# Kernel tuning notes

Measured on AMD Instinct MI355X. Metric: run time of the kernel, lower is better.

The kernel has to match this reference:

```python
import jax, jax.numpy as jnp
import numpy as np

HIDDEN = 1024
VOCAB = 32000
MAX_LENGTH = 30
SOS_TOKEN = 0


def setup_inputs() -> dict:
    key = jax.random.key(0)
    ks = jax.random.split(key, 10)
    B = 64
    s = 1.0 / np.sqrt(HIDDEN)
    return {
        "encoder_outputs": jax.random.normal(ks[0], (B, MAX_LENGTH, HIDDEN), jnp.float32),
        "encoder_hidden": jax.random.normal(ks[1], (1, B, HIDDEN), jnp.float32),
        "target_tensor": jax.random.randint(ks[2], (B, MAX_LENGTH), 0, VOCAB),
        "embedding": jax.random.normal(ks[3], (VOCAB, HIDDEN), jnp.float32),
        "w_ih": jax.random.uniform(ks[4], (3 * HIDDEN, HIDDEN), jnp.float32, -s, s),
        "w_hh": jax.random.uniform(ks[5], (3 * HIDDEN, HIDDEN), jnp.float32, -s, s),
        "b_ih": jax.random.uniform(ks[6], (3 * HIDDEN,), jnp.float32, -s, s),
        "b_hh": jax.random.uniform(ks[7], (3 * HIDDEN,), jnp.float32, -s, s),
        "out_w": jax.random.uniform(ks[8], (VOCAB, HIDDEN), jnp.float32, -s, s),
        "out_b": jax.random.uniform(ks[9], (VOCAB,), jnp.float32, -s, s),
    }


def reference(encoder_outputs, encoder_hidden, target_tensor, embedding,
              w_ih, w_hh, b_ih, b_hh, out_w, out_b):
    B = encoder_outputs.shape[0]
    h0 = encoder_hidden[0]  # [B, H]
    # teacher forcing: step i consumes SOS for i=0, else target[:, i-1]
    sos = jnp.full((B, 1), SOS_TOKEN, dtype=target_tensor.dtype)
    tokens = jnp.concatenate([sos, target_tensor[:, :-1]], axis=1).T  # [T, B]

    def step(h, tok):
        x = jax.nn.relu(embedding[tok])            # [B, H] (dropout = identity in eval)
        gi = x @ w_ih.T + b_ih                     # [B, 3H]
        gh = h @ w_hh.T + b_hh                     # [B, 3H]
        i_r, i_z, i_n = jnp.split(gi, 3, axis=-1)
        h_r, h_z, h_n = jnp.split(gh, 3, axis=-1)
        r = jax.nn.sigmoid(i_r + h_r)
        z = jax.nn.sigmoid(i_z + h_z)
        n = jnp.tanh(i_n + r * h_n)
        h_new = (1.0 - z) * n + z * h
        logits = h_new @ out_w.T + out_b           # [B, V]
        return h_new, logits

    h_final, logits = jax.lax.scan(step, h0, tokens)   # logits: [T, B, V]
    log_probs = jax.nn.log_softmax(logits.transpose(1, 0, 2), axis=-1)  # [B, T, V]
    return log_probs, h_final[None]  # hidden as [1, B, H]
```

## Files before the change

### kernel.cpp

```cpp
#include <hip/hip_runtime.h>
#include <math.h>

#define T_STEPS 30
#define BATCH   64
#define HID     1024
#define VOCABN  32000
#define G3      3072
#define ROWS    (T_STEPS * BATCH)
#define ROWS_PAD 2048
#define OUT_HID_OFF ((size_t)BATCH * T_STEPS * VOCABN)

typedef __attribute__((ext_vector_type(8))) short bf16x8;
typedef __attribute__((ext_vector_type(4))) float f32x4;

__device__ __forceinline__ unsigned short f2bf(float f) {
    union { float f; unsigned u; } x; x.f = f;
    unsigned r = x.u + 0x7fffu + ((x.u >> 16) & 1u);
    return (unsigned short)(r >> 16);
}
__device__ __forceinline__ float bf2f(unsigned short u) {
    union { unsigned u; float f; } x; x.u = (unsigned)u << 16;
    return x.f;
}

__device__ __forceinline__ void gld_lds16(const unsigned short* g, unsigned short* l) {
    __builtin_amdgcn_global_load_lds(
        (const __attribute__((address_space(1))) unsigned*)g,
        (__attribute__((address_space(3))) unsigned*)l, 16, 0, 0);
}

__global__ __launch_bounds__(256) void f32_to_bf16(const float* __restrict__ src,
                                                   unsigned short* __restrict__ dst, int n4) {
    int i = blockIdx.x * 256 + threadIdx.x;
    int stride = gridDim.x * 256;
    for (; i < n4; i += stride) {
        float4 v = ((const float4*)src)[i];
        ushort4 o;
        o.x = f2bf(v.x); o.y = f2bf(v.y); o.z = f2bf(v.z); o.w = f2bf(v.w);
        ((ushort4*)dst)[i] = o;
    }
}

__global__ __launch_bounds__(256) void embed_relu_bf16(const int* __restrict__ target,
                                                       const float* __restrict__ emb,
                                                       unsigned short* __restrict__ X) {
    int bid = blockIdx.x;
    int t = bid >> 6, b = bid & 63;
    int tok = (t == 0) ? 0 : target[b * T_STEPS + (t - 1)];
    const float4* src = (const float4*)(emb + (size_t)tok * HID);
    float4 v = src[threadIdx.x];
    ushort4 o;
    o.x = f2bf(fmaxf(v.x, 0.f)); o.y = f2bf(fmaxf(v.y, 0.f));
    o.z = f2bf(fmaxf(v.z, 0.f)); o.w = f2bf(fmaxf(v.w, 0.f));
    ((ushort4*)(X + (size_t)bid * HID))[threadIdx.x] = o;
}

__global__ void init_bar(unsigned int* bar) {
    if (threadIdx.x < 64) bar[threadIdx.x] = 0u;
}

__global__ __launch_bounds__(256) void gemm_mfma_bt(const unsigned short* __restrict__ A,
                                                    const unsigned short* __restrict__ W,
                                                    const float* __restrict__ bias,
                                                    float* __restrict__ out,
                                                    int N, int K) {
    __shared__ unsigned short As[128 * 64];
    __shared__ unsigned short Bs[128 * 64];
    int tid  = threadIdx.x;
    int lane = tid & 63;
    int wid  = tid >> 6;
    int wm   = wid >> 1, wn = wid & 1;
    const int bM = blockIdx.y * 128;
    const int bN = blockIdx.x * 128;

    f32x4 acc[4][4];
#pragma unroll
    for (int i = 0; i < 4; ++i)
#pragma unroll
        for (int j = 0; j < 4; ++j) acc[i][j] = (f32x4){0.f, 0.f, 0.f, 0.f};

    int sr[4], sc[4];
#pragma unroll
    for (int q = 0; q < 4; ++q) {
        sr[q] = (wid * 4 + q) * 8 + (lane >> 3);
        sc[q] = (lane & 7) ^ (sr[q] & 7);
    }

    for (int kt = 0; kt < K; kt += 64) {
        __syncthreads();
#pragma unroll
        for (int q = 0; q < 4; ++q) {
            gld_lds16(A + (size_t)(bM + sr[q]) * K + kt + sc[q] * 8, As + (wid * 4 + q) * 512);
            gld_lds16(W + (size_t)(bN + sr[q]) * K + kt + sc[q] * 8, Bs + (wid * 4 + q) * 512);
        }
        __syncthreads();

#pragma unroll
        for (int ks = 0; ks < 2; ++ks) {
            bf16x8 a[4], b[4];
#pragma unroll
            for (int mf = 0; mf < 4; ++mf) {
                int r  = wm * 64 + mf * 16 + (lane & 15);
                int ch = (ks * 4 + (lane >> 4)) ^ (r & 7);
                a[mf] = *(const bf16x8*)(As + r * 64 + ch * 8);
            }
#pragma unroll
            for (int nf = 0; nf < 4; ++nf) {
                int r  = wn * 64 + nf * 16 + (lane & 15);
                int ch = (ks * 4 + (lane >> 4)) ^ (r & 7);
                b[nf] = *(const bf16x8*)(Bs + r * 64 + ch * 8);
            }
#pragma unroll
            for (int mf = 0; mf < 4; ++mf)
#pragma unroll
                for (int nf = 0; nf < 4; ++nf)
                    acc[mf][nf] = __builtin_amdgcn_mfma_f32_16x16x32_bf16(
                        a[mf], b[nf], acc[mf][nf], 0, 0, 0);
        }
    }

    int rif = (lane >> 4) * 4;
    int col = lane & 15;
#pragma unroll
    for (int mf = 0; mf < 4; ++mf) {
#pragma unroll
        for (int j = 0; j < 4; ++j) {
            int gr = bM + wm * 64 + mf * 16 + rif + j;
#pragma unroll
            for (int nf = 0; nf < 4; ++nf) {
                int gc = bN + wn * 64 + nf * 16 + col;
                out[(size_t)gr * N + gc] = acc[mf][nf][j] + bias[gc];
            }
        }
    }
}

template <bool BF16OUT>
__global__ __launch_bounds__(512) void gemm_logits256(const unsigned short* __restrict__ A,
                                                      const unsigned short* __restrict__ W,
                                                      const float* __restrict__ bias,
                                                      float* __restrict__ out,
                                                      unsigned short* __restrict__ scratch) {
    __shared__ unsigned short As[2][256 * 32];
    __shared__ unsigned short Bs[2][256 * 32];
    int d   = blockIdx.x;
    int xcd = d & 7;
    int mt  = (d >> 3) & 7;
    int pg  = d >> 6;
    int p   = pg * 8 + xcd;
    if (p >= VOCABN / 256) return;
    const int bM = mt * 256;
    const int bN = p * 256;

    int tid  = threadIdx.x;
    int lane = tid & 63;
    int wid  = tid >> 6;
    int wm   = wid >> 2;
    int wn   = wid & 3;
    int l15  = lane & 15, l4 = lane >> 4;

    size_t pA[2], pB[2];
    int ldst[2];
#pragma unroll
    for (int i = 0; i < 2; ++i) {
        int c = wid * 128 + i * 64 + lane;
        int r = c >> 2, cc = c & 3;
        int so = (cc ^ ((r >> 1) & 3)) * 8;
        pA[i] = (size_t)(bM + r) * HID + so;
        pB[i] = (size_t)(bN + r) * HID + so;
        ldst[i] = wid * 1024 + i * 512;
    }

    f32x4 acc[8][4];
#pragma unroll
    for (int i = 0; i < 8; ++i)
#pragma unroll
        for (int j = 0; j < 4; ++j) acc[i][j] = (f32x4){0.f, 0.f, 0.f, 0.f};

    int chsw = (l4 ^ ((l15 >> 1) & 3)) * 8;
    int aoff[8], boff[4];
#pragma unroll
    for (int mf = 0; mf < 8; ++mf) aoff[mf] = (wm * 128 + mf * 16 + l15) * 32 + chsw;
#pragma unroll
    for (int nf = 0; nf < 4; ++nf) boff[nf] = (wn * 64 + nf * 16 + l15) * 32 + chsw;

    auto issue = [&](int s) {
        int slot = s & 1;
#pragma unroll
        for (int i = 0; i < 2; ++i)
            gld_lds16(A + pA[i] + s * 32, &As[slot][ldst[i]]);
#pragma unroll
        for (int i = 0; i < 2; ++i)
            gld_lds16(W + pB[i] + s * 32, &Bs[slot][ldst[i]]);
    };

    issue(0); issue(1);

#pragma unroll 1
    for (int s = 0; s < 32; ++s) {
        if (s < 31) asm volatile("s_waitcnt vmcnt(4)" ::: "memory");
        else        asm volatile("s_waitcnt vmcnt(0)" ::: "memory");
        __builtin_amdgcn_s_barrier();
        asm volatile("" ::: "memory");
        __builtin_amdgcn_sched_barrier(0);

        int slot = s & 1;
        const unsigned short* ab = As[slot];
        const unsigned short* bb = Bs[slot];
        bf16x8 a[8], b[4];
#pragma unroll
        for (int mf = 0; mf < 8; ++mf) a[mf] = *(const bf16x8*)(ab + aoff[mf]);
#pragma unroll
        for (int nf = 0; nf < 4; ++nf) b[nf] = *(const bf16x8*)(bb + boff[nf]);
        __builtin_amdgcn_s_setprio(1);
#pragma unroll
        for (int mf = 0; mf < 8; ++mf)
#pragma unroll
            for (int nf = 0; nf < 4; ++nf)
                acc[mf][nf] = __builtin_amdgcn_mfma_f32_16x16x32_bf16(
                    a[mf], b[nf], acc[mf][nf], 0, 0, 0);
        __builtin_amdgcn_s_setprio(0);

        asm volatile("s_waitcnt lgkmcnt(0)" ::: "memory");
        __builtin_amdgcn_s_barrier();
        asm volatile("" ::: "memory");
        __builtin_amdgcn_sched_barrier(0);
        if (s < 30) issue(s + 2);
    }

    int col = l15;
    float b4[4];
#pragma unroll
    for (int nf = 0; nf < 4; ++nf) b4[nf] = bias[bN + wn * 64 + nf * 16 + col];
    int rif = l4 * 4;
#pragma unroll
    for (int mf = 0; mf < 8; ++mf) {
#pragma unroll
        for (int j = 0; j < 4; ++j) {
            int gr = bM + wm * 128 + mf * 16 + rif + j;
            if (gr < ROWS) {
                int t = gr >> 6, b_ = gr & 63;
                size_t rowoff = ((size_t)b_ * T_STEPS + t) * (size_t)VOCABN;
#pragma unroll
                for (int nf = 0; nf < 4; ++nf) {
                    float v = acc[mf][nf][j] + b4[nf];
                    int gc = bN + wn * 64 + nf * 16 + col;
                    if (BF16OUT) scratch[rowoff + gc] = f2bf(v);
                    else         out[rowoff + gc] = v;
                }
            }
        }
    }
}

__global__ __launch_bounds__(256, 1) void gru_persistent(
    const unsigned short* __restrict__ h0b,
    const float* __restrict__ enc_h,
    const unsigned short* __restrict__ Whh,
    const float* __restrict__ b_hh,
    const float* __restrict__ gi,
    unsigned short* __restrict__ Hall,
    float* __restrict__ h_final,
    unsigned int* __restrict__ flags,
    const float* __restrict__ outw_f32,
    unsigned short* __restrict__ outw_bf)
{
    __shared__ unsigned short Wlds[48 * 1024];
    int tid  = threadIdx.x;

    if (blockIdx.x >= 64) {
        const int n4 = VOCABN * HID / 4;
        int i = (blockIdx.x - 64) * 256 + tid;
        const int stride = 192 * 256;
        for (; i < n4; i += stride) {
            float4 v = ((const float4*)outw_f32)[i];
            ushort4 o;
            o.x = f2bf(v.x); o.y = f2bf(v.y); o.z = f2bf(v.z); o.w = f2bf(v.w);
            ((ushort4*)outw_bf)[i] = o;
        }
        return;
    }

    int lane = tid & 63;
    int wq   = tid >> 6;
    int l15  = lane & 15, l4 = lane >> 4;
    int m0   = blockIdx.x * 16;
    int b    = wq * 16 + l15;
    int mb   = m0 + l4 * 4;

    for (int i = 0; i < 24; ++i) {
        int sb = wq * 24 + i;
        int kt = sb / 3, g = sb % 3;
        const unsigned short* src =
            Whh + (size_t)(g * HID + m0 + l15) * HID + kt * 32 + l4 * 8;
        gld_lds16(src, Wlds + sb * 512);
    }

    float hp[4];
    {
        float4 h4 = *(const float4*)(enc_h + (size_t)b * HID + mb);
        hp[0] = h4.x; hp[1] = h4.y; hp[2] = h4.z; hp[3] = h4.w;
    }
    float bhr[4], bhz[4], bhn[4];
    {
        float4 r4 = *(const float4*)(b_hh + mb);
        float4 z4 = *(const float4*)(b_hh + HID + mb);
        float4 n4 = *(const float4*)(b_hh + 2 * HID + mb);
        bhr[0]=r4.x; bhr[1]=r4.y; bhr[2]=r4.z; bhr[3]=r4.w;
        bhz[0]=z4.x; bhz[1]=z4.y; bhz[2]=z4.z; bhz[3]=z4.w;
        bhn[0]=n4.x; bhn[1]=n4.y; bhn[2]=n4.z; bhn[3]=n4.w;
    }
    __syncthreads();

    int arow16 = b * 128 + l4;

    for (int t = 0; t < T_STEPS; ++t) {
        const float* gib = gi + (size_t)t * BATCH * G3 + (size_t)b * G3;
        float4 giR = *(const float4*)(gib + mb);
        float4 giZ = *(const float4*)(gib + HID + mb);
        float4 giN = *(const float4*)(gib + 2 * HID + mb);
        float gr4[4] = {giR.x, giR.y, giR.z, giR.w};
        float gz4[4] = {giZ.x, giZ.y, giZ.z, giZ.w};
        float gn4[4] = {giN.x, giN.y, giN.z, giN.w};

        if (t > 0) {
            if (tid < 64) {
                while (__hip_atomic_load(flags + tid, __ATOMIC_RELAXED,
                                         __HIP_MEMORY_SCOPE_AGENT) < (unsigned)t) {}
            }
            __builtin_amdgcn_sched_barrier(0);
            __syncthreads();
            asm volatile("" ::: "memory");
        }

        const unsigned short* Asrc = (t == 0) ? h0b : (Hall + (size_t)(t - 1) * BATCH * HID);
        const bf16x8* A16 = (const bf16x8*)Asrc;

        bf16x8 hreg[32];
#pragma unroll
        for (int kt = 0; kt < 32; ++kt) hreg[kt] = A16[arow16 + kt * 4];

        f32x4 acc[3];
#pragma unroll
        for (int g = 0; g < 3; ++g) acc[g] = (f32x4){0.f, 0.f, 0.f, 0.f};

#pragma unroll
        for (int kt = 0; kt < 32; ++kt) {
#pragma unroll
            for (int g = 0; g < 3; ++g) {
                bf16x8 wfrag = *(const bf16x8*)(Wlds + ((size_t)(kt * 3 + g) * 64 + lane) * 8);
                acc[g] = __builtin_amdgcn_mfma_f32_16x16x32_bf16(wfrag, hreg[kt], acc[g], 0, 0, 0);
            }
        }

        unsigned long long pack = 0;
#pragma unroll
        for (int j = 0; j < 4; ++j) {
            float r = 1.f / (1.f + __expf(-(gr4[j] + acc[0][j] + bhr[j])));
            float z = 1.f / (1.f + __expf(-(gz4[j] + acc[1][j] + bhz[j])));
            float e2 = __expf(2.f * (gn4[j] + r * (acc[2][j] + bhn[j])));
            float n = 1.f - 2.f / (e2 + 1.f);
            float hnew = (1.f - z) * n + z * hp[j];
            hp[j] = hnew;
            pack |= (unsigned long long)f2bf(hnew) << (16 * j);
        }
        __hip_atomic_store((unsigned long long*)(Hall + (size_t)t * BATCH * HID +
                                                 (size_t)b * HID + mb),
                           pack, __ATOMIC_RELAXED, __HIP_MEMORY_SCOPE_AGENT);
        if (t == T_STEPS - 1) {
            float4 hf = {hp[0], hp[1], hp[2], hp[3]};
            *(float4*)(h_final + (size_t)b * HID + mb) = hf;
        }

        if (t < T_STEPS - 1) {
            __syncthreads();
            if (tid == 0)
                __hip_atomic_store(flags + blockIdx.x, (unsigned)(t + 1),
                                   __ATOMIC_RELAXED, __HIP_MEMORY_SCOPE_AGENT);
        }
    }
}

__global__ __launch_bounds__(256) void lsm_fused_bf16(const unsigned short* __restrict__ scratch,
                                                      float* __restrict__ out) {
    __shared__ bf16x8 srow[4000];
    __shared__ float2 sred[4];
    __shared__ float sc;
    const bf16x8* src = (const bf16x8*)(scratch + (size_t)blockIdx.x * VOCABN);
    float* dst = out + (size_t)blockIdx.x * VOCABN;
    int tid = threadIdx.x;
    int lane = tid & 63, w = tid >> 6;

    float m = -1e30f, s = 0.f;
    for (int i = tid; i < 4000; i += 256) {
        bf16x8 v = src[i];
        srow[i] = v;
        float f[8];
#pragma unroll
        for (int j = 0; j < 8; ++j) f[j] = bf2f((unsigned short)v[j]);
        float cm = f[0];
#pragma unroll
        for (int j = 1; j < 8; ++j) cm = fmaxf(cm, f[j]);
        if (cm > m) { s *= __expf(m - cm); m = cm; }
#pragma unroll
        for (int j = 0; j < 8; ++j) s += __expf(f[j] - m);
    }
#pragma unroll
    for (int off = 1; off < 64; off <<= 1) {
        float om = __shfl_xor(m, off, 64);
        float os = __shfl_xor(s, off, 64);
        float nm = fmaxf(m, om);
        s = s * __expf(m - nm) + os * __expf(om - nm);
        m = nm;
    }
    if (lane == 0) sred[w] = make_float2(m, s);
    __syncthreads();
    if (tid == 0) {
        float fm = sred[0].x, fs = sred[0].y;
#pragma unroll
        for (int k = 1; k < 4; ++k) {
            float om = sred[k].x, os = sred[k].y;
            float nm = fmaxf(fm, om);
            fs = fs * __expf(fm - nm) + os * __expf(om - nm);
            fm = nm;
        }
        sc = fm + logf(fs);
    }
    __syncthreads();
    float c = sc;
    for (int i = tid; i < 4000; i += 256) {
        bf16x8 v = srow[i];
        float4 o0, o1;
        o0.x = bf2f((unsigned short)v[0]) - c; o0.y = bf2f((unsigned short)v[1]) - c;
        o0.z = bf2f((unsigned short)v[2]) - c; o0.w = bf2f((unsigned short)v[3]) - c;
        o1.x = bf2f((unsigned short)v[4]) - c; o1.y = bf2f((unsigned short)v[5]) - c;
        o1.z = bf2f((unsigned short)v[6]) - c; o1.w = bf2f((unsigned short)v[7]) - c;
        ((float4*)dst)[i * 2] = o0;
        ((float4*)dst)[i * 2 + 1] = o1;
    }
}

__global__ __launch_bounds__(256) void lsm_fused(float* __restrict__ out) {
    float4* p4 = (float4*)(out + (size_t)blockIdx.x * VOCABN);
    int tid = threadIdx.x;
    int lane = tid & 63, w = tid >> 6;
    __shared__ float2 sred[4];
    __shared__ float sc;

    float m = -1e30f, s = 0.f;
    for (int i = tid; i < VOCABN / 4; i += 256) {
        float4 v = p4[i];
        float cm = fmaxf(fmaxf(v.x, v.y), fmaxf(v.z, v.w));
        if (cm > m) { s *= __expf(m - cm); m = cm; }
        s += __expf(v.x - m) + __expf(v.y - m) + __expf(v.z - m) + __expf(v.w - m);
    }
#pragma unroll
    for (int off = 1; off < 64; off <<= 1) {
        float om = __shfl_xor(m, off, 64);
        float os = __shfl_xor(s, off, 64);
        float nm = fmaxf(m, om);
        s = s * __expf(m - nm) + os * __expf(om - nm);
        m = nm;
    }
    if (lane == 0) sred[w] = make_float2(m, s);
    __syncthreads();
    if (tid == 0) {
        float fm = sred[0].x, fs = sred[0].y;
#pragma unroll
        for (int k = 1; k < 4; ++k) {
            float om = sred[k].x, os = sred[k].y;
            float nm = fmaxf(fm, om);
            fs = fs * __expf(fm - nm) + os * __expf(om - nm);
            fm = nm;
        }
        sc = fm + logf(fs);
    }
    __syncthreads();
    float c = sc;
    for (int i = tid; i < VOCABN / 4; i += 256) {
        float4 v = p4[i];
        v.x -= c; v.y -= c; v.z -= c; v.w -= c;
        p4[i] = v;
    }
}

extern "C" void kernel_launch(void* const* d_in, const int* in_sizes, int n_in,
                              void* d_out, int out_size, void* d_ws, size_t ws_size,
                              hipStream_t stream) {
    const float* enc_h  = (const float*)d_in[1];
    const int*   target = (const int*)d_in[2];
    const float* emb    = (const float*)d_in[3];
    const float* w_ih   = (const float*)d_in[4];
    const float* w_hh   = (const float*)d_in[5];
    const float* b_ih   = (const float*)d_in[6];
    const float* b_hh   = (const float*)d_in[7];
    const float* out_w  = (const float*)d_in[8];
    const float* out_b  = (const float*)d_in[9];
    float* out = (float*)d_out;

    char* p0 = (char*)d_ws;
    char* p = p0;
    unsigned short* Xb   = (unsigned short*)p; p += (size_t)ROWS * HID * 2;
    unsigned short* Wih  = (unsigned short*)p; p += (size_t)G3 * HID * 2;
    unsigned short* OutW = (unsigned short*)p; p += (size_t)VOCABN * HID * 2;
    unsigned short* Hall = (unsigned short*)p; p += (size_t)ROWS_PAD * HID * 2;
    float* gi   = (float*)p; p += (size_t)ROWS * G3 * 4;
    unsigned short* Whhb = (unsigned short*)p; p += (size_t)G3 * HID * 2;
    unsigned short* h0b  = (unsigned short*)p; p += (size_t)BATCH * HID * 2;
    unsigned int* bar = (unsigned int*)p; p += 256 * sizeof(unsigned int);
    unsigned short* lscratch = (unsigned short*)p; p += (size_t)ROWS * VOCABN * 2;
    const bool use_bf16 = ((size_t)(p - p0) <= ws_size);

    f32_to_bf16<<<768, 256, 0, stream>>>(w_ih, Wih, G3 * HID / 4);
    f32_to_bf16<<<768, 256, 0, stream>>>(w_hh, Whhb, G3 * HID / 4);
    f32_to_bf16<<<64, 256, 0, stream>>>(enc_h, h0b, BATCH * HID / 4);
    embed_relu_bf16<<<ROWS, 256, 0, stream>>>(target, emb, Xb);
    init_bar<<<1, 64, 0, stream>>>(bar);

    gemm_mfma_bt<<<dim3(G3 / 128, ROWS / 128), 256, 0, stream>>>(Xb, Wih, b_ih, gi, G3, HID);

    {
        const unsigned short* a0 = h0b;
        const float* a1 = enc_h;
        const unsigned short* a2 = Whhb;
        const float* a3 = b_hh;
        const float* a4 = gi;
        unsigned short* a5 = Hall;
        float* a6 = out + OUT_HID_OFF;
        unsigned int* a7 = bar;
        const float* a8 = out_w;
        unsigned short* a9 = OutW;
        void* args[] = {&a0, &a1, &a2, &a3, &a4, &a5, &a6, &a7, &a8, &a9};
        hipLaunchCooperativeKernel((void*)gru_persistent, dim3(256), dim3(256),
                                   args, 0, stream);
    }

    if (use_bf16) {
        gemm_logits256<true><<<1024, 512, 0, stream>>>(Hall, OutW, out_b, out, lscratch);
        lsm_fused_bf16<<<ROWS, 256, 0, stream>>>(lscratch, out);
    } else {
        gemm_logits256<false><<<1024, 512, 0, stream>>>(Hall, OutW, out_b, out, nullptr);
        lsm_fused<<<ROWS, 256, 0, stream>>>(out);
    }
}
```

Baseline: 499.9 us.

## Fuse GRU recurrence and logits GEMM into one cooperative kernel with work queue

Merges the persistent GRU kernel and the logits GEMM into a single cooperative kernel of 512-thread blocks. Blocks claim logits tiles from an atomic counter and spin on per-step GRU flags, so row-tiles whose timesteps are finished can start before the recurrence ends. This is meant to hide the serial GRU latency and remove a kernel launch. The trade-offs are that the GRU blocks now leave half their waves idle, the tile GEMM shares LDS with the GRU weights, and spin-waiting plus dynamic scheduling adds overhead and deadlock risk.

```diff
diff --git a/kernel.cpp b/kernel.cpp
--- a/kernel.cpp
+++ b/kernel.cpp
@@ -9,6 +9,7 @@
 #define ROWS    (T_STEPS * BATCH)
 #define ROWS_PAD 2048
 #define OUT_HID_OFF ((size_t)BATCH * T_STEPS * VOCABN)
+#define N_ITEMS 1000
 
 typedef __attribute__((ext_vector_type(8))) short bf16x8;
 typedef __attribute__((ext_vector_type(4))) float f32x4;
@@ -56,7 +57,7 @@
 }
 
 __global__ void init_bar(unsigned int* bar) {
-    if (threadIdx.x < 64) bar[threadIdx.x] = 0u;
+    if (threadIdx.x < 128) bar[threadIdx.x] = 0u;
 }
 
 __global__ __launch_bounds__(256) void gemm_mfma_bt(const unsigned short* __restrict__ A,
@@ -136,22 +137,15 @@
 }
 
 template <bool BF16OUT>
-__global__ __launch_bounds__(512) void gemm_logits256(const unsigned short* __restrict__ A,
-                                                      const unsigned short* __restrict__ W,
-                                                      const float* __restrict__ bias,
-                                                      float* __restrict__ out,
-                                                      unsigned short* __restrict__ scratch) {
-    __shared__ unsigned short As[2][256 * 32];
-    __shared__ unsigned short Bs[2][256 * 32];
-    int d   = blockIdx.x;
-    int xcd = d & 7;
-    int mt  = (d >> 3) & 7;
-    int pg  = d >> 6;
-    int p   = pg * 8 + xcd;
-    if (p >= VOCABN / 256) return;
+__device__ void gemm_tile(int mt, int p,
+                          const unsigned short* __restrict__ A,
+                          const unsigned short* __restrict__ W,
+                          const float* __restrict__ bias,
+                          float* __restrict__ out,
+                          unsigned short* __restrict__ scratch,
+                          unsigned short* AsB, unsigned short* BsB) {
     const int bM = mt * 256;
     const int bN = p * 256;
-
     int tid  = threadIdx.x;
     int lane = tid & 63;
     int wid  = tid >> 6;
@@ -188,10 +182,10 @@
         int slot = s & 1;
 #pragma unroll
         for (int i = 0; i < 2; ++i)
-            gld_lds16(A + pA[i] + s * 32, &As[slot][ldst[i]]);
+            gld_lds16(A + pA[i] + s * 32, AsB + slot * 8192 + ldst[i]);
 #pragma unroll
         for (int i = 0; i < 2; ++i)
-            gld_lds16(W + pB[i] + s * 32, &Bs[slot][ldst[i]]);
+            gld_lds16(W + pB[i] + s * 32, BsB + slot * 8192 + ldst[i]);
     };
 
     issue(0); issue(1);
@@ -205,8 +199,8 @@
         __builtin_amdgcn_sched_barrier(0);
 
         int slot = s & 1;
-        const unsigned short* ab = As[slot];
-        const unsigned short* bb = Bs[slot];
+        const unsigned short* ab = AsB + slot * 8192;
+        const unsigned short* bb = BsB + slot * 8192;
         bf16x8 a[8], b[4];
 #pragma unroll
         for (int mf = 0; mf < 8; ++mf) a[mf] = *(const bf16x8*)(ab + aoff[mf]);
@@ -253,7 +247,8 @@
     }
 }
 
-__global__ __launch_bounds__(256, 1) void gru_persistent(
+template <bool BF16OUT>
+__global__ __launch_bounds__(512, 1) void fused_coop(
     const unsigned short* __restrict__ h0b,
     const float* __restrict__ enc_h,
     const unsigned short* __restrict__ Whh,
@@ -262,122 +257,171 @@
     unsigned short* __restrict__ Hall,
     float* __restrict__ h_final,
     unsigned int* __restrict__ flags,
+    unsigned int* __restrict__ ctr,
     const float* __restrict__ outw_f32,
-    unsigned short* __restrict__ outw_bf)
+    unsigned short* __restrict__ outw_bf,
+    const float* __restrict__ out_b,
+    float* __restrict__ out,
+    unsigned short* __restrict__ lscratch)
 {
-    __shared__ unsigned short Wlds[48 * 1024];
+    __shared__ unsigned short smem[48 * 1024];
+    __shared__ int sitem;
     int tid  = threadIdx.x;
-
-    if (blockIdx.x >= 64) {
-        const int n4 = VOCABN * HID / 4;
-        int i = (blockIdx.x - 64) * 256 + tid;
-        const int stride = 192 * 256;
-        for (; i < n4; i += stride) {
+    int bidx = blockIdx.x;
+
+    if (bidx >= 64) {
+        const int n8 = VOCABN * HID / 4;
+        int i = (bidx - 64) * 512 + tid;
+        const int stride = 192 * 512;
+        for (; i < n8; i += stride) {
             float4 v = ((const float4*)outw_f32)[i];
-            ushort4 o;
-            o.x = f2bf(v.x); o.y = f2bf(v.y); o.z = f2bf(v.z); o.w = f2bf(v.w);
-            ((ushort4*)outw_bf)[i] = o;
-        }
-        return;
-    }
-
-    int lane = tid & 63;
-    int wq   = tid >> 6;
-    int l15  = lane & 15, l4 = lane >> 4;
-    int m0   = blockIdx.x * 16;
-    int b    = wq * 16 + l15;
-    int mb   = m0 + l4 * 4;
-
-    for (int i = 0; i < 24; ++i) {
-        int sb = wq * 24 + i;
-        int kt = sb / 3, g = sb % 3;
-        const unsigned short* src =
-            Whh + (size_t)(g * HID + m0 + l15) * HID + kt * 32 + l4 * 8;
-        gld_lds16(src, Wlds + sb * 512);
-    }
-
-    float hp[4];
-    {
-        float4 h4 = *(const float4*)(enc_h + (size_t)b * HID + mb);
-        hp[0] = h4.x; hp[1] = h4.y; hp[2] = h4.z; hp[3] = h4.w;
-    }
-    float bhr[4], bhz[4], bhn[4];
-    {
-        float4 r4 = *(const float4*)(b_hh + mb);
-        float4 z4 = *(const float4*)(b_hh + HID + mb);
-        float4 n4 = *(const float4*)(b_hh + 2 * HID + mb);
-        bhr[0]=r4.x; bhr[1]=r4.y; bhr[2]=r4.z; bhr[3]=r4.w;
-        bhz[0]=z4.x; bhz[1]=z4.y; bhz[2]=z4.z; bhz[3]=z4.w;
-        bhn[0]=n4.x; bhn[1]=n4.y; bhn[2]=n4.z; bhn[3]=n4.w;
-    }
-    __syncthreads();
-
-    int arow16 = b * 128 + l4;
-
-    for (int t = 0; t < T_STEPS; ++t) {
-        const float* gib = gi + (size_t)t * BATCH * G3 + (size_t)b * G3;
-        float4 giR = *(const float4*)(gib + mb);
-        float4 giZ = *(const float4*)(gib + HID + mb);
-        float4 giN = *(const float4*)(gib + 2 * HID + mb);
-        float gr4[4] = {giR.x, giR.y, giR.z, giR.w};
-        float gz4[4] = {giZ.x, giZ.y, giZ.z, giZ.w};
-        float gn4[4] = {giN.x, giN.y, giN.z, giN.w};
-
-        if (t > 0) {
-            if (tid < 64) {
-                while (__hip_atomic_load(flags + tid, __ATOMIC_RELAXED,
-                                         __HIP_MEMORY_SCOPE_AGENT) < (unsigned)t) {}
-            }
-            __builtin_amdgcn_sched_barrier(0);
-            __syncthreads();
-            asm volatile("" ::: "memory");
-        }
-
-        const unsigned short* Asrc = (t == 0) ? h0b : (Hall + (size_t)(t - 1) * BATCH * HID);
-        const bf16x8* A16 = (const bf16x8*)Asrc;
-
-        bf16x8 hreg[32];
-#pragma unroll
-        for (int kt = 0; kt < 32; ++kt) hreg[kt] = A16[arow16 + kt * 4];
-
-        f32x4 acc[3];
-#pragma unroll
-        for (int g = 0; g < 3; ++g) acc[g] = (f32x4){0.f, 0.f, 0.f, 0.f};
-
-#pragma unroll
-        for (int kt = 0; kt < 32; ++kt) {
-#pragma unroll
-            for (int g = 0; g < 3; ++g) {
-                bf16x8 wfrag = *(const bf16x8*)(Wlds + ((size_t)(kt * 3 + g) * 64 + lane) * 8);
-                acc[g] = __builtin_amdgcn_mfma_f32_16x16x32_bf16(wfrag, hreg[kt], acc[g], 0, 0, 0);
-            }
-        }
-
-        unsigned long long pack = 0;
-#pragma unroll
-        for (int j = 0; j < 4; ++j) {
-            float r = 1.f / (1.f + __expf(-(gr4[j] + acc[0][j] + bhr[j])));
-            float z = 1.f / (1.f + __expf(-(gz4[j] + acc[1][j] + bhz[j])));
-            float e2 = __expf(2.f * (gn4[j] + r * (acc[2][j] + bhn[j])));
-            float n = 1.f - 2.f / (e2 + 1.f);
-            float hnew = (1.f - z) * n + z * hp[j];
-            hp[j] = hnew;
-            pack |= (unsigned long long)f2bf(hnew) << (16 * j);
-        }
-        __hip_atomic_store((unsigned long long*)(Hall + (size_t)t * BATCH * HID +
-                                                 (size_t)b * HID + mb),
-                           pack, __ATOMIC_RELAXED, __HIP_MEMORY_SCOPE_AGENT);
-        if (t == T_STEPS - 1) {
-            float4 hf = {hp[0], hp[1], hp[2], hp[3]};
-            *(float4*)(h_final + (size_t)b * HID + mb) = hf;
-        }
-
-        if (t < T_STEPS - 1) {
+            unsigned long long pk =
+                (unsigned long long)f2bf(v.x) |
+                ((unsigned long long)f2bf(v.y) << 16) |
+                ((unsigned long long)f2bf(v.z) << 32) |
+                ((unsigned long long)f2bf(v.w) << 48);
+            __hip_atomic_store((unsigned long long*)outw_bf + i, pk,
+                               __ATOMIC_RELAXED, __HIP_MEMORY_SCOPE_AGENT);
+        }
+        __syncthreads();
+        if (tid == 0)
+            __hip_atomic_fetch_add(ctr + 1, 1u, __ATOMIC_RELAXED,
+                                   __HIP_MEMORY_SCOPE_AGENT);
+    } else {
+        int lane = tid & 63;
+        int wq   = tid >> 6;
+        bool act = (wq < 4);
+        int l15  = lane & 15, l4 = lane >> 4;
+        int m0   = bidx * 16;
+        int b    = (wq & 3) * 16 + l15;
+        int mb   = m0 + l4 * 4;
+
+        if (act) {
+            for (int i = 0; i < 24; ++i) {
+                int sb = wq * 24 + i;
+                int kt = sb / 3, g = sb % 3;
+                const unsigned short* src =
+                    Whh + (size_t)(g * HID + m0 + l15) * HID + kt * 32 + l4 * 8;
+                gld_lds16(src, smem + sb * 512);
+            }
+        }
+
+        float hp[4] = {0.f, 0.f, 0.f, 0.f};
+        float bhr[4], bhz[4], bhn[4];
+        if (act) {
+            float4 h4 = *(const float4*)(enc_h + (size_t)b * HID + mb);
+            hp[0] = h4.x; hp[1] = h4.y; hp[2] = h4.z; hp[3] = h4.w;
+            float4 r4 = *(const float4*)(b_hh + mb);
+            float4 z4 = *(const float4*)(b_hh + HID + mb);
+            float4 n4 = *(const float4*)(b_hh + 2 * HID + mb);
+            bhr[0]=r4.x; bhr[1]=r4.y; bhr[2]=r4.z; bhr[3]=r4.w;
+            bhz[0]=z4.x; bhz[1]=z4.y; bhz[2]=z4.z; bhz[3]=z4.w;
+            bhn[0]=n4.x; bhn[1]=n4.y; bhn[2]=n4.z; bhn[3]=n4.w;
+        }
+        __syncthreads();
+
+        int arow16 = b * 128 + l4;
+
+        for (int t = 0; t < T_STEPS; ++t) {
+            float gr4[4], gz4[4], gn4[4];
+            if (act) {
+                const float* gib = gi + (size_t)t * BATCH * G3 + (size_t)b * G3;
+                float4 giR = *(const float4*)(gib + mb);
+                float4 giZ = *(const float4*)(gib + HID + mb);
+                float4 giN = *(const float4*)(gib + 2 * HID + mb);
+                gr4[0]=giR.x; gr4[1]=giR.y; gr4[2]=giR.z; gr4[3]=giR.w;
+                gz4[0]=giZ.x; gz4[1]=giZ.y; gz4[2]=giZ.z; gz4[3]=giZ.w;
+                gn4[0]=giN.x; gn4[1]=giN.y; gn4[2]=giN.z; gn4[3]=giN.w;
+            }
+
+            if (t > 0) {
+                if (tid < 64) {
+                    while (__hip_atomic_load(flags + tid, __ATOMIC_RELAXED,
+                                             __HIP_MEMORY_SCOPE_AGENT) < (unsigned)t) {}
+                }
+                __builtin_amdgcn_sched_barrier(0);
+                __syncthreads();
+                asm volatile("" ::: "memory");
+            }
+
+            if (act) {
+                const unsigned short* Asrc =
+                    (t == 0) ? h0b : (Hall + (size_t)(t - 1) * BATCH * HID);
+                const bf16x8* A16 = (const bf16x8*)Asrc;
+
+                bf16x8 hreg[32];
+#pragma unroll
+                for (int kt = 0; kt < 32; ++kt) hreg[kt] = A16[arow16 + kt * 4];
+
+                f32x4 acc[3];
+#pragma unroll
+                for (int g = 0; g < 3; ++g) acc[g] = (f32x4){0.f, 0.f, 0.f, 0.f};
+
+#pragma unroll
+                for (int kt = 0; kt < 32; ++kt) {
+#pragma unroll
+                    for (int g = 0; g < 3; ++g) {
+                        bf16x8 wfrag =
+                            *(const bf16x8*)(smem + ((size_t)(kt * 3 + g) * 64 + lane) * 8);
+                        acc[g] = __builtin_amdgcn_mfma_f32_16x16x32_bf16(
+                            wfrag, hreg[kt], acc[g], 0, 0, 0);
+                    }
+                }
+
+                unsigned long long pack = 0;
+#pragma unroll
+                for (int j = 0; j < 4; ++j) {
+                    float r = 1.f / (1.f + __expf(-(gr4[j] + acc[0][j] + bhr[j])));
+                    float z = 1.f / (1.f + __expf(-(gz4[j] + acc[1][j] + bhz[j])));
+                    float e2 = __expf(2.f * (gn4[j] + r * (acc[2][j] + bhn[j])));
+                    float n = 1.f - 2.f / (e2 + 1.f);
+                    float hnew = (1.f - z) * n + z * hp[j];
+                    hp[j] = hnew;
+                    pack |= (unsigned long long)f2bf(hnew) << (16 * j);
+                }
+                __hip_atomic_store((unsigned long long*)(Hall + (size_t)t * BATCH * HID +
+                                                         (size_t)b * HID + mb),
+                                   pack, __ATOMIC_RELAXED, __HIP_MEMORY_SCOPE_AGENT);
+                if (t == T_STEPS - 1) {
+                    float4 hf = {hp[0], hp[1], hp[2], hp[3]};
+                    *(float4*)(h_final + (size_t)b * HID + mb) = hf;
+                }
+            }
+
             __syncthreads();
             if (tid == 0)
-                __hip_atomic_store(flags + blockIdx.x, (unsigned)(t + 1),
+                __hip_atomic_store(flags + bidx, (unsigned)(t + 1),
                                    __ATOMIC_RELAXED, __HIP_MEMORY_SCOPE_AGENT);
         }
+    }
+
+    if (tid == 0) {
+        while (__hip_atomic_load(ctr + 1, __ATOMIC_RELAXED,
+                                 __HIP_MEMORY_SCOPE_AGENT) < 192u) {}
+    }
+    __builtin_amdgcn_sched_barrier(0);
+    __syncthreads();
+    asm volatile("" ::: "memory");
+
+    for (;;) {
+        __syncthreads();
+        if (tid == 0) sitem = (int)atomicAdd(ctr, 1u);
+        __syncthreads();
+        int item = sitem;
+        if (item >= N_ITEMS) break;
+        int mt = item / 125;
+        int p  = item - mt * 125;
+        unsigned need = (unsigned)(mt * 4 + 4);
+        if (need > 30u) need = 30u;
+        if (tid < 64) {
+            while (__hip_atomic_load(flags + tid, __ATOMIC_RELAXED,
+                                     __HIP_MEMORY_SCOPE_AGENT) < need) {}
+        }
+        __builtin_amdgcn_sched_barrier(0);
+        __syncthreads();
+        asm volatile("" ::: "memory");
+        gemm_tile<BF16OUT>(mt, p, Hall, outw_bf, out_b, out, lscratch,
+                           smem, smem + 16384);
     }
 }
 
@@ -510,12 +554,13 @@
     unsigned int* bar = (unsigned int*)p; p += 256 * sizeof(unsigned int);
     unsigned short* lscratch = (unsigned short*)p; p += (size_t)ROWS * VOCABN * 2;
     const bool use_bf16 = ((size_t)(p - p0) <= ws_size);
+    unsigned int* ctr = bar + 64;
 
     f32_to_bf16<<<768, 256, 0, stream>>>(w_ih, Wih, G3 * HID / 4);
     f32_to_bf16<<<768, 256, 0, stream>>>(w_hh, Whhb, G3 * HID / 4);
     f32_to_bf16<<<64, 256, 0, stream>>>(enc_h, h0b, BATCH * HID / 4);
     embed_relu_bf16<<<ROWS, 256, 0, stream>>>(target, emb, Xb);
-    init_bar<<<1, 64, 0, stream>>>(bar);
+    init_bar<<<1, 128, 0, stream>>>(bar);
 
     gemm_mfma_bt<<<dim3(G3 / 128, ROWS / 128), 256, 0, stream>>>(Xb, Wih, b_ih, gi, G3, HID);
 
@@ -528,18 +573,22 @@
         unsigned short* a5 = Hall;
         float* a6 = out + OUT_HID_OFF;
         unsigned int* a7 = bar;
-        const float* a8 = out_w;
-        unsigned short* a9 = OutW;
-        void* args[] = {&a0, &a1, &a2, &a3, &a4, &a5, &a6, &a7, &a8, &a9};
-        hipLaunchCooperativeKernel((void*)gru_persistent, dim3(256), dim3(256),
-                                   args, 0, stream);
-    }
-
-    if (use_bf16) {
-        gemm_logits256<true><<<1024, 512, 0, stream>>>(Hall, OutW, out_b, out, lscratch);
-        lsm_fused_bf16<<<ROWS, 256, 0, stream>>>(lscratch, out);
-    } else {
-        gemm_logits256<false><<<1024, 512, 0, stream>>>(Hall, OutW, out_b, out, nullptr);
-        lsm_fused<<<ROWS, 256, 0, stream>>>(out);
-    }
-}
+        unsigned int* a8 = ctr;
+        const float* a9 = out_w;
+        unsigned short* a10 = OutW;
+        const float* a11 = out_b;
+        float* a12 = out;
+        unsigned short* a13 = lscratch;
+        void* args[] = {&a0, &a1, &a2, &a3, &a4, &a5, &a6, &a7, &a8,
+                        &a9, &a10, &a11, &a12, &a13};
+        if (use_bf16)
+            hipLaunchCooperativeKernel((void*)fused_coop<true>, dim3(256), dim3(512),
+                                       args, 0, stream);
+        else
+            hipLaunchCooperativeKernel((void*)fused_coop<false>, dim3(256), dim3(512),
+                                       args, 0, stream);
+    }
+
+    if (use_bf16) lsm_fused_bf16<<<ROWS, 256, 0, stream>>>(lscratch, out);
+    else          lsm_fused<<<ROWS, 256, 0, stream>>>(out);
+}
```

After: 442.4 us, median of 2. 1.13x faster.
